# Kernel optimization log

Hardware: AMD Instinct MI355X
Metric: run time of the kernel (lower is better)

The kernel has to match this reference:

```python
import jax, jax.numpy as jnp
import numpy as np

N_NODES = 50000


def _gcn_conv(x, W, b, src, dst, norm, n_nodes):
    # x: [N, Fin], W: [Fin, Fout]
    h = x @ W                                   # [N, Fout]
    msg = h[src] * norm[:, None]                # [E+N, Fout] edge messages
    out = jax.ops.segment_sum(msg, dst, num_segments=n_nodes)
    return out + b


def reference(x, edge_index, W1, b1, W2, b2):
    n = x.shape[0]
    # add self-loops (PyG GCNConv default add_self_loops=True)
    loop = jnp.arange(n, dtype=edge_index.dtype)
    src = jnp.concatenate([edge_index[0], loop])
    dst = jnp.concatenate([edge_index[1], loop])
    # symmetric degree normalization: deg over destination with unit weights
    deg = jax.ops.segment_sum(jnp.ones_like(dst, dtype=x.dtype), dst, num_segments=n)
    dinv = jnp.where(deg > 0, jax.lax.rsqrt(deg), 0.0)
    norm = dinv[src] * dinv[dst]                # [E+N]
    h = _gcn_conv(x, W1, b1, src, dst, norm, n)
    h = jax.nn.relu(h)
    out = _gcn_conv(h, W2, b2, src, dst, norm, n)
    return out


def setup_inputs() -> dict:
    key = jax.random.key(0)
    k1, k2, k3, k4 = jax.random.split(key, 4)
    n, e, fin, hid, fout = N_NODES, 800000, 128, 128, 64
    x = jax.random.normal(k1, (n, fin), dtype=jnp.float32)
    edge_index = jax.random.randint(k2, (2, e), 0, n, dtype=jnp.int64)
    # Glorot-ish init for linear weights, zero bias (PyG default)
    W1 = jax.random.normal(k3, (fin, hid), dtype=jnp.float32) / np.sqrt(fin)
    b1 = jnp.zeros((hid,), dtype=jnp.float32)
    W2 = jax.random.normal(k4, (hid, fout), dtype=jnp.float32) / np.sqrt(hid)
    b2 = jnp.zeros((fout,), dtype=jnp.float32)
    return {"x": x, "edge_index": edge_index, "W1": W1, "b1": b1, "W2": W2, "b2": b2}
```

## Files before the change

### kernel.cpp

```cpp
#include <hip/hip_runtime.h>
#include <hip/hip_bf16.h>


constexpr int FIN = 128;
constexpr int HID = 128;
constexpr int FOUT = 64;
constexpr int CAP = 48;
constexpr int NPB = 98;
constexpr int BCAP = 3072;
constexpr int OVF_MAX = 65536;

typedef __attribute__((ext_vector_type(8))) short s16x8;
typedef __attribute__((ext_vector_type(4))) float f32x4;

static __device__ __forceinline__ float bf2f(__hip_bfloat16 v) { return __bfloat162float(v); }
static __device__ __forceinline__ float lo2f(unsigned u) { union { unsigned i; float f; } c; c.i = u << 16; return c.f; }
static __device__ __forceinline__ float hi2f(unsigned u) { union { unsigned i; float f; } c; c.i = u & 0xffff0000u; return c.f; }
static __device__ __forceinline__ unsigned short f2bfu(float f) {
    __hip_bfloat16 h = __float2bfloat16(f);
    union { __hip_bfloat16 h; unsigned short u; } c; c.h = h; return c.u;
}
static __device__ __forceinline__ unsigned pack2(float a, float b) {
    return (unsigned)f2bfu(a) | ((unsigned)f2bfu(b) << 16);
}
static __device__ __forceinline__ void acc_add(float* acc, uint4 v) {
    acc[0] += lo2f(v.x); acc[1] += hi2f(v.x);
    acc[2] += lo2f(v.y); acc[3] += hi2f(v.y);
    acc[4] += lo2f(v.z); acc[5] += hi2f(v.z);
    acc[6] += lo2f(v.w); acc[7] += hi2f(v.w);
}
static __device__ __forceinline__ void acc_fma(float* acc, uint4 v, float w) {
    acc[0] += w * lo2f(v.x); acc[1] += w * hi2f(v.x);
    acc[2] += w * lo2f(v.y); acc[3] += w * hi2f(v.y);
    acc[4] += w * lo2f(v.z); acc[5] += w * hi2f(v.z);
    acc[6] += w * lo2f(v.w); acc[7] += w * hi2f(v.w);
}

struct SW { int s; float w; };

__global__ __launch_bounds__(256) void k_detect(const unsigned* __restrict__ xw,
                                                const int* __restrict__ eiw,
                                                int E, int* __restrict__ flags,
                                                int* __restrict__ gcur,
                                                int* __restrict__ cnt, int N, int zero_cnt) {
    if (zero_cnt)
        for (long i = (long)blockIdx.x * 256 + threadIdx.x; i < N; i += (long)gridDim.x * 256)
            cnt[i] = 0;
    if (blockIdx.x != 0) return;
    for (int i = threadIdx.x; i < 514; i += 256) gcur[i] = 0;
    __shared__ int s_bf16like, s_oddnz;
    if (threadIdx.x == 0) { s_bf16like = 0; s_oddnz = 0; }
    __syncthreads();
    int c = 0;
    for (int i = threadIdx.x; i < 4096; i += 256) {
        unsigned ex = ((xw[i] & 0xffffu) >> 7) & 0xffu;
        if (ex >= 117u && ex <= 130u) c++;
    }
    atomicAdd(&s_bf16like, c);
    int nz = 0;
    for (int i = threadIdx.x; i < 2048; i += 256)
        if (eiw[2 * i + 1] != 0) nz++;
    atomicAdd(&s_oddnz, nz);
    __syncthreads();
    if (threadIdx.x == 0) {
        flags[0] = (s_bf16like < 2048) ? 1 : 0;
        flags[1] = (s_oddnz == 0) ? 1 : 0;
    }
}

__global__ __launch_bounds__(256) void k_mega(const void* __restrict__ Xp,
                                              const void* __restrict__ Wp,
                                              const int* __restrict__ ei, int E, int N,
                                              int nbuk, int GB,
                                              int* __restrict__ gcur,
                                              unsigned* __restrict__ pairs,
                                              int2* __restrict__ ovfA,
                                              int* __restrict__ ovfAcnt,
                                              __hip_bfloat16* __restrict__ G,
                                              const int* __restrict__ flags) {
    extern __shared__ __align__(16) char smem[];
    const int tid = threadIdx.x;
    if ((int)blockIdx.x < GB) {
        short* Wt = (short*)smem;
        const bool f32m = flags[0] != 0;
        for (int i = tid; i < 128 * 128; i += 256) {
            int k = i >> 7, n = i & 127;
            float wv = f32m ? ((const float*)Wp)[(long)k * 128 + n]
                            : bf2f(((const __hip_bfloat16*)Wp)[(long)k * 128 + n]);
            Wt[n * 136 + k] = (short)f2bfu(wv);
        }
        __syncthreads();
        const int w = tid >> 6, lane = tid & 63;
        const int m = lane & 15, quad = lane >> 4;
        const int rowA = blockIdx.x * 64 + w * 16 + m;
        const int rowc = rowA < N ? rowA : N - 1;
        s16x8 afr[4];
#pragma unroll
        for (int kc = 0; kc < 4; ++kc) {
            const int k0 = kc * 32 + quad * 8;
            if (!f32m) {
                afr[kc] = *(const s16x8*)((const __hip_bfloat16*)Xp + (long)rowc * 128 + k0);
            } else {
                const float* p = (const float*)Xp + (long)rowc * 128 + k0;
                s16x8 t;
#pragma unroll
                for (int j = 0; j < 8; ++j) t[j] = (short)f2bfu(p[j]);
                afr[kc] = t;
            }
        }
        const int rbase = blockIdx.x * 64 + w * 16 + quad * 4;
#pragma unroll
        for (int ct = 0; ct < 8; ++ct) {
            f32x4 acc = {0.f, 0.f, 0.f, 0.f};
#pragma unroll
            for (int kc = 0; kc < 4; ++kc) {
                s16x8 bfr = *(const s16x8*)&Wt[(ct * 16 + m) * 136 + kc * 32 + quad * 8];
                acc = __builtin_amdgcn_mfma_f32_16x16x32_bf16(afr[kc], bfr, acc, 0, 0, 0);
            }
            const int plane = ct >> 2;
            const int cp = (ct & 3) * 16 + m;
#pragma unroll
            for (int r = 0; r < 4; ++r) {
                int rr = rbase + r;
                if (rr < N)
                    G[(long)plane * N * 64 + (long)rr * 64 + cp] = __float2bfloat16(acc[r]);
            }
        }
    } else {
        int* hist = (int*)smem;
        int* gbase = hist + 512;
        const long base = (long)(blockIdx.x - GB) * 2048;
        const bool i64 = flags[1] != 0;
        int se[8], de[8];
        for (int b = tid; b < nbuk; b += 256) hist[b] = 0;
        __syncthreads();
#pragma unroll
        for (int j = 0; j < 8; ++j) {
            long i = base + j * 256 + tid;
            int s = 0, d = -1;
            if (i < E) {
                if (i64) { s = ((const int2*)ei)[i].x; d = ((const int2*)(ei + 2 * (long)E))[i].x; }
                else     { s = ei[i]; d = ei[(long)E + i]; }
                if ((unsigned)s >= (unsigned)N || (unsigned)d >= (unsigned)N) d = -1;
            }
            se[j] = s; de[j] = d;
            if (d >= 0) atomicAdd(&hist[d / NPB], 1);
        }
        __syncthreads();
        for (int b = tid; b < nbuk; b += 256) {
            int h = hist[b];
            gbase[b] = h > 0 ? atomicAdd(&gcur[b], h) : 0;
            hist[b] = 0;
        }
        __syncthreads();
#pragma unroll
        for (int j = 0; j < 8; ++j) {
            int d = de[j];
            if (d < 0) continue;
            int b = d / NPB;
            int p = gbase[b] + atomicAdd(&hist[b], 1);
            if (p < BCAP) {
                pairs[(long)b * BCAP + p] = ((unsigned)(d - b * NPB) << 16) | (unsigned)se[j];
            } else {
                int op = atomicAdd(ovfAcnt, 1);
                if (op < OVF_MAX) ovfA[op] = make_int2(d, se[j]);
            }
        }
    }
}

__global__ __launch_bounds__(256) void k_binB(const int* __restrict__ gcur,
                                              const unsigned* __restrict__ pairs,
                                              const int2* __restrict__ ovfA,
                                              const int* __restrict__ ovfAcnt,
                                              int* __restrict__ cnt,
                                              float* __restrict__ dinv,
                                              unsigned short* __restrict__ slots,
                                              int2* __restrict__ ovf2,
                                              int* __restrict__ ovf2cnt, int N) {
    __shared__ int cntL[NPB];
    __shared__ __align__(16) unsigned short slotsL[NPB * CAP];
    const int b = blockIdx.x;
    const int tid = threadIdx.x;
    const int d0 = b * NPB;
    const int nd = min(NPB, N - d0);
    if (nd <= 0) return;
    for (int i = tid; i < NPB; i += 256) cntL[i] = 0;
    __syncthreads();
    const int c = min(gcur[b], BCAP);
    const unsigned* pb = pairs + (long)b * BCAP;
    for (int i = tid; i < c; i += 256) {
        unsigned p = pb[i];
        int ld = p >> 16;
        int pos = atomicAdd(&cntL[ld], 1);
        if (pos < CAP) {
            slotsL[ld * CAP + pos] = (unsigned short)(p & 0xffffu);
        } else {
            int op = atomicAdd(ovf2cnt, 1);
            if (op < OVF_MAX) ovf2[op] = make_int2(d0 + ld, (int)(p & 0xffffu));
        }
    }
    int na = *ovfAcnt; na = na < OVF_MAX ? na : OVF_MAX;
    for (int i = tid; i < na; i += 256) {
        int2 p = ovfA[i];
        int ld = p.x - d0;
        if ((unsigned)ld < (unsigned)nd) {
            int pos = atomicAdd(&cntL[ld], 1);
            if (pos < CAP) {
                slotsL[ld * CAP + pos] = (unsigned short)p.y;
            } else {
                int op = atomicAdd(ovf2cnt, 1);
                if (op < OVF_MAX) ovf2[op] = p;
            }
        }
    }
    __syncthreads();
    for (int i = tid; i < nd; i += 256) {
        cnt[d0 + i] = cntL[i];
        dinv[d0 + i] = rsqrtf((float)(cntL[i] + 1));
    }
    const uint4* sv = (const uint4*)slotsL;
    uint4* gv = (uint4*)(slots + (long)d0 * CAP);
    const int total8 = (nd * CAP) >> 3;
    for (int i = tid; i < total8; i += 256) gv[i] = sv[i];
}

__global__ __launch_bounds__(256) void k_build_direct(const int* __restrict__ ei, int E, int N,
                                                      int* __restrict__ cnt,
                                                      int* __restrict__ slots,
                                                      int2* __restrict__ ovf2,
                                                      int* __restrict__ ovf2cnt,
                                                      const int* __restrict__ flags) {
    long i = (long)blockIdx.x * 256 + threadIdx.x;
    if (i >= E) return;
    int s, d;
    if (flags[1]) { s = ((const int2*)ei)[i].x; d = ((const int2*)(ei + 2 * (long)E))[i].x; }
    else          { s = ei[i]; d = ei[(long)E + i]; }
    if ((unsigned)s >= (unsigned)N || (unsigned)d >= (unsigned)N) return;
    int pos = atomicAdd(&cnt[d], 1);
    if (pos < CAP) {
        slots[(long)d * CAP + pos] = s;
    } else {
        int op = atomicAdd(ovf2cnt, 1);
        if (op < OVF_MAX) ovf2[op] = make_int2(d, s);
    }
}

template<int CT, int SPLIT>
__global__ __launch_bounds__(256) void k_gemm(const void* __restrict__ Xp, int x_follows_flag,
                                              const void* __restrict__ Wp,
                                              const int* __restrict__ cnt,
                                              __hip_bfloat16* __restrict__ G,
                                              const int* __restrict__ flags, int N) {
    constexpr int C = CT * 16;
    __shared__ __align__(16) short Wt[C * 136];
    const bool f32m = flags[0] != 0;
    const bool xf32 = (x_follows_flag != 0) && f32m;
    const int tid = threadIdx.x;
    for (int i = tid; i < 128 * C; i += 256) {
        int k = i / C, n = i % C;
        float wv = f32m ? ((const float*)Wp)[(long)k * C + n]
                        : bf2f(((const __hip_bfloat16*)Wp)[(long)k * C + n]);
        Wt[n * 136 + k] = (short)f2bfu(wv);
    }
    __syncthreads();
    const int w = tid >> 6, lane = tid & 63;
    const int m = lane & 15, quad = lane >> 4;
    const int rowA = blockIdx.x * 64 + w * 16 + m;
    const int rowc = rowA < N ? rowA : N - 1;
    s16x8 afr[4];
#pragma unroll
    for (int kc = 0; kc < 4; ++kc) {
        const int k0 = kc * 32 + quad * 8;
        if (!xf32) {
            afr[kc] = *(const s16x8*)((const __hip_bfloat16*)Xp + (long)rowc * 128 + k0);
        } else {
            const float* p = (const float*)Xp + (long)rowc * 128 + k0;
            s16x8 t;
#pragma unroll
            for (int j = 0; j < 8; ++j) t[j] = (short)f2bfu(p[j]);
            afr[kc] = t;
        }
    }
    const int rbase = blockIdx.x * 64 + w * 16 + quad * 4;
    float dv[4];
#pragma unroll
    for (int r = 0; r < 4; ++r) {
        int rr = min(rbase + r, N - 1);
        dv[r] = rsqrtf((float)(cnt[rr] + 1));
    }
#pragma unroll
    for (int ct = 0; ct < CT; ++ct) {
        f32x4 acc = {0.f, 0.f, 0.f, 0.f};
#pragma unroll
        for (int kc = 0; kc < 4; ++kc) {
            s16x8 bfr = *(const s16x8*)&Wt[(ct * 16 + m) * 136 + kc * 32 + quad * 8];
            acc = __builtin_amdgcn_mfma_f32_16x16x32_bf16(afr[kc], bfr, acc, 0, 0, 0);
        }
#pragma unroll
        for (int r = 0; r < 4; ++r) {
            int rr = rbase + r;
            if (rr < N) {
                long off;
                if (SPLIT) {
                    const int plane = ct / (CT / 2);
                    const int cp = (ct % (CT / 2)) * 16 + m;
                    off = (long)plane * N * (C / 2) + (long)rr * (C / 2) + cp;
                } else {
                    off = (long)rr * C + ct * 16 + m;
                }
                G[off] = __float2bfloat16(dv[r] * acc[r]);
            }
        }
    }
}

__global__ __launch_bounds__(256) void k_gather1b(const __hip_bfloat16* __restrict__ G,
                                                  const int* __restrict__ cnt,
                                                  const float* __restrict__ dinv,
                                                  const unsigned short* __restrict__ slots,
                                                  const int2* __restrict__ ovf2,
                                                  const int* __restrict__ ovf2cnt,
                                                  const void* __restrict__ b1,
                                                  __hip_bfloat16* __restrict__ h1,
                                                  const int* __restrict__ flags, int N) {
    __shared__ int cntL[32];
    __shared__ float wsL[32];
    __shared__ __align__(16) SW swL[32 * 49];
    const int tid = threadIdx.x;
    const int n0 = blockIdx.x * 32;
    const int nd = min(32, N - n0);
    for (int i = tid; i < nd; i += 256) {
        cntL[i] = cnt[n0 + i];
        wsL[i] = dinv[n0 + i];
    }
    __syncthreads();
    for (int j = tid; j < 32 * CAP; j += 256) {
        const int ni = j / CAP, sl = j - ni * CAP;
        if (ni < nd) {
            const int mm = min(cntL[ni], CAP);
            if (sl < mm) {
                const int s = slots[(long)(n0 + ni) * CAP + sl];
                swL[ni * 49 + sl].s = s;
                swL[ni * 49 + sl].w = dinv[s];
            }
        }
    }
    __syncthreads();
    const int grp = tid >> 3, lane = tid & 7;
    if (grp >= nd) return;
    const int node = n0 + grp;
    const int cd = cntL[grp];
    const int m = cd < CAP ? cd : CAP;
    const float wself = wsL[grp];
    const SW* sw = &swL[grp * 49];
    const bool f32m = flags[0] != 0;
    for (int P = 0; P < 2; ++P) {
        const __hip_bfloat16* Gp = G + (long)P * N * 64;
        float acc[8] = {0, 0, 0, 0, 0, 0, 0, 0};
        acc_fma(acc, ((const uint4*)(Gp + (long)node * 64))[lane], wself);
        int i = 0;
        for (; i + 7 < m; i += 8) {
            SW a0 = sw[i], a1 = sw[i + 1], a2 = sw[i + 2], a3 = sw[i + 3];
            SW a4 = sw[i + 4], a5 = sw[i + 5], a6 = sw[i + 6], a7 = sw[i + 7];
            uint4 v0 = ((const uint4*)(Gp + (long)a0.s * 64))[lane];
            uint4 v1 = ((const uint4*)(Gp + (long)a1.s * 64))[lane];
            uint4 v2 = ((const uint4*)(Gp + (long)a2.s * 64))[lane];
            uint4 v3 = ((const uint4*)(Gp + (long)a3.s * 64))[lane];
            uint4 v4 = ((const uint4*)(Gp + (long)a4.s * 64))[lane];
            uint4 v5 = ((const uint4*)(Gp + (long)a5.s * 64))[lane];
            uint4 v6 = ((const uint4*)(Gp + (long)a6.s * 64))[lane];
            uint4 v7 = ((const uint4*)(Gp + (long)a7.s * 64))[lane];
            acc_fma(acc, v0, a0.w); acc_fma(acc, v1, a1.w);
            acc_fma(acc, v2, a2.w); acc_fma(acc, v3, a3.w);
            acc_fma(acc, v4, a4.w); acc_fma(acc, v5, a5.w);
            acc_fma(acc, v6, a6.w); acc_fma(acc, v7, a7.w);
        }
        for (; i + 3 < m; i += 4) {
            SW a0 = sw[i], a1 = sw[i + 1], a2 = sw[i + 2], a3 = sw[i + 3];
            uint4 v0 = ((const uint4*)(Gp + (long)a0.s * 64))[lane];
            uint4 v1 = ((const uint4*)(Gp + (long)a1.s * 64))[lane];
            uint4 v2 = ((const uint4*)(Gp + (long)a2.s * 64))[lane];
            uint4 v3 = ((const uint4*)(Gp + (long)a3.s * 64))[lane];
            acc_fma(acc, v0, a0.w); acc_fma(acc, v1, a1.w);
            acc_fma(acc, v2, a2.w); acc_fma(acc, v3, a3.w);
        }
        for (; i < m; ++i) {
            SW a = sw[i];
            acc_fma(acc, ((const uint4*)(Gp + (long)a.s * 64))[lane], a.w);
        }
        if (cd > CAP) {
            int oc = *ovf2cnt; oc = oc < OVF_MAX ? oc : OVF_MAX;
            for (int j = 0; j < oc; ++j)
                if (ovf2[j].x == node) {
                    int s0 = ovf2[j].y;
                    acc_fma(acc, ((const uint4*)(Gp + (long)s0 * 64))[lane], dinv[s0]);
                }
        }
        const int c0 = P * 64 + lane * 8;
        float bv[8];
        if (f32m) {
            const float4* bp = (const float4*)((const float*)b1 + c0);
            float4 b0 = bp[0], b1v = bp[1];
            bv[0] = b0.x; bv[1] = b0.y; bv[2] = b0.z; bv[3] = b0.w;
            bv[4] = b1v.x; bv[5] = b1v.y; bv[6] = b1v.z; bv[7] = b1v.w;
        } else {
            uint4 b = *(const uint4*)((const __hip_bfloat16*)b1 + c0);
            bv[0] = lo2f(b.x); bv[1] = hi2f(b.x); bv[2] = lo2f(b.y); bv[3] = hi2f(b.y);
            bv[4] = lo2f(b.z); bv[5] = hi2f(b.z); bv[6] = lo2f(b.w); bv[7] = hi2f(b.w);
        }
        float o[8];
#pragma unroll
        for (int c = 0; c < 8; ++c) {
            float v = wself * acc[c] + bv[c];
            o[c] = v > 0.f ? v : 0.f;
        }
        uint4 pv = { pack2(o[0], o[1]), pack2(o[2], o[3]), pack2(o[4], o[5]), pack2(o[6], o[7]) };
        ((uint4*)(h1 + (long)node * 128 + P * 64))[lane] = pv;
    }
}

template<int F, int LAYER1, typename ST>
__global__ __launch_bounds__(256) void k_gather(const __hip_bfloat16* __restrict__ G,
                                                const int* __restrict__ cnt,
                                                const ST* __restrict__ slots,
                                                const int2* __restrict__ ovf2,
                                                const int* __restrict__ ovf2cnt,
                                                const void* __restrict__ bias,
                                                void* __restrict__ outp,
                                                const int* __restrict__ flags, int N) {
    constexpr int L = F / 8;
    constexpr int NODES = 256 / L;
    const int tid = threadIdx.x;
    const int grp = tid / L, lane = tid % L;
    const int node = blockIdx.x * NODES + grp;
    if (node >= N) return;
    const int cd = cnt[node];
    const float wself = rsqrtf((float)(cd + 1));
    const int m = cd < CAP ? cd : CAP;
    const ST* sl = slots + (long)node * CAP;
    float acc[8] = {0, 0, 0, 0, 0, 0, 0, 0};
    acc_add(acc, ((const uint4*)(G + (long)node * F))[lane]);
    int i = 0;
    for (; i + 7 < m; i += 8) {
        int s0 = sl[i], s1 = sl[i + 1], s2 = sl[i + 2], s3 = sl[i + 3];
        int s4 = sl[i + 4], s5 = sl[i + 5], s6 = sl[i + 6], s7 = sl[i + 7];
        uint4 v0 = ((const uint4*)(G + (long)s0 * F))[lane];
        uint4 v1 = ((const uint4*)(G + (long)s1 * F))[lane];
        uint4 v2 = ((const uint4*)(G + (long)s2 * F))[lane];
        uint4 v3 = ((const uint4*)(G + (long)s3 * F))[lane];
        uint4 v4 = ((const uint4*)(G + (long)s4 * F))[lane];
        uint4 v5 = ((const uint4*)(G + (long)s5 * F))[lane];
        uint4 v6 = ((const uint4*)(G + (long)s6 * F))[lane];
        uint4 v7 = ((const uint4*)(G + (long)s7 * F))[lane];
        acc_add(acc, v0); acc_add(acc, v1); acc_add(acc, v2); acc_add(acc, v3);
        acc_add(acc, v4); acc_add(acc, v5); acc_add(acc, v6); acc_add(acc, v7);
    }
    for (; i + 3 < m; i += 4) {
        int s0 = sl[i], s1 = sl[i + 1], s2 = sl[i + 2], s3 = sl[i + 3];
        uint4 v0 = ((const uint4*)(G + (long)s0 * F))[lane];
        uint4 v1 = ((const uint4*)(G + (long)s1 * F))[lane];
        uint4 v2 = ((const uint4*)(G + (long)s2 * F))[lane];
        uint4 v3 = ((const uint4*)(G + (long)s3 * F))[lane];
        acc_add(acc, v0); acc_add(acc, v1); acc_add(acc, v2); acc_add(acc, v3);
    }
    for (; i < m; ++i)
        acc_add(acc, ((const uint4*)(G + (long)sl[i] * F))[lane]);
    if (cd > CAP) {
        int oc = *ovf2cnt; oc = oc < OVF_MAX ? oc : OVF_MAX;
        for (int j = 0; j < oc; ++j)
            if (ovf2[j].x == node)
                acc_add(acc, ((const uint4*)(G + (long)ovf2[j].y * F))[lane]);
    }
    const bool f32m = flags[0] != 0;
    const int c0 = lane * 8;
    float bv[8];
    if (f32m) {
        const float4* bp = (const float4*)((const float*)bias + c0);
        float4 b0 = bp[0], b1 = bp[1];
        bv[0] = b0.x; bv[1] = b0.y; bv[2] = b0.z; bv[3] = b0.w;
        bv[4] = b1.x; bv[5] = b1.y; bv[6] = b1.z; bv[7] = b1.w;
    } else {
        uint4 b = *(const uint4*)((const __hip_bfloat16*)bias + c0);
        bv[0] = lo2f(b.x); bv[1] = hi2f(b.x); bv[2] = lo2f(b.y); bv[3] = hi2f(b.y);
        bv[4] = lo2f(b.z); bv[5] = hi2f(b.z); bv[6] = lo2f(b.w); bv[7] = hi2f(b.w);
    }
    float o[8];
#pragma unroll
    for (int c = 0; c < 8; ++c) {
        float v = wself * acc[c] + bv[c];
        o[c] = (LAYER1 && v < 0.f) ? 0.f : v;
    }
    if (LAYER1 || !f32m) {
        uint4 pv = { pack2(o[0], o[1]), pack2(o[2], o[3]), pack2(o[4], o[5]), pack2(o[6], o[7]) };
        ((uint4*)outp)[(long)node * L + lane] = pv;
    } else {
        float4* op = (float4*)((float*)outp + (long)node * F + c0);
        op[0] = make_float4(o[0], o[1], o[2], o[3]);
        op[1] = make_float4(o[4], o[5], o[6], o[7]);
    }
}

extern "C" void kernel_launch(void* const* d_in, const int* in_sizes, int n_in,
                              void* d_out, int out_size, void* d_ws, size_t ws_size,
                              hipStream_t stream) {
    const void* x  = d_in[0];
    const int*  ei = (const int*)d_in[1];
    const void* W1 = d_in[2];
    const void* b1 = d_in[3];
    const void* W2 = d_in[4];
    const void* b2 = d_in[5];

    const int N = in_sizes[0] / FIN;
    const int E = in_sizes[1] / 2;
    const int nbuk = (N + NPB - 1) / NPB;

    char* ws = (char*)d_ws;
    int*   flags   = (int*)ws;
    int*   gcur    = (int*)(ws + 4096);
    int*   ovfAcnt = gcur + 512;
    int*   ovf2cnt = gcur + 513;
    int*   cnt     = (int*)(ws + 65536);
    float* dinv    = (float*)(ws + 266240);
    int2*  ovfA    = (int2*)(ws + 524288);
    int2*  ovf2    = (int2*)(ws + 1048576);
    unsigned short* slots16 = (unsigned short*)(ws + 2097152);
    int*   slots32 = (int*)(ws + 2097152);
    __hip_bfloat16* g  = (__hip_bfloat16*)(ws + 11730944);
    __hip_bfloat16* g2 = g;
    unsigned* pairs = (unsigned*)(ws + 24530944);
    __hip_bfloat16* h1 = (__hip_bfloat16*)(ws + 24530944);

    const int GB = (N + 63) / 64;
    const int AB = (E + 2047) / 2048;
    const int EB = (E + 255) / 256;

    if (N <= 65536 && nbuk <= 512) {
        k_detect<<<1, 256, 0, stream>>>((const unsigned*)x, ei, E, flags, gcur, cnt, N, 0);
        k_mega<<<GB + AB, 256, 34816, stream>>>(x, W1, ei, E, N, nbuk, GB,
                                                gcur, pairs, ovfA, ovfAcnt, g, flags);
        k_binB<<<nbuk, 256, 0, stream>>>(gcur, pairs, ovfA, ovfAcnt, cnt, dinv, slots16, ovf2, ovf2cnt, N);
        const int GBL = (N + 31) / 32;
        k_gather1b<<<GBL, 256, 0, stream>>>(g, cnt, dinv, slots16, ovf2, ovf2cnt, b1, h1, flags, N);
        k_gemm<4, 0><<<GB, 256, 0, stream>>>(h1, 0, W2, cnt, g2, flags, N);
        k_gather<64, 0, unsigned short><<<(N + 31) / 32, 256, 0, stream>>>(
            g2, cnt, slots16, ovf2, ovf2cnt, b2, d_out, flags, N);
    } else {
        k_detect<<<64, 256, 0, stream>>>((const unsigned*)x, ei, E, flags, gcur, cnt, N, 1);
        k_build_direct<<<EB, 256, 0, stream>>>(ei, E, N, cnt, slots32, ovf2, ovf2cnt, flags);
        k_gemm<8, 0><<<GB, 256, 0, stream>>>(x, 1, W1, cnt, g, flags, N);
        k_gather<128, 1, int><<<(N + 15) / 16, 256, 0, stream>>>(
            g, cnt, slots32, ovf2, ovf2cnt, b1, h1, flags, N);
        k_gemm<4, 0><<<GB, 256, 0, stream>>>(h1, 0, W2, cnt, g2, flags, N);
        k_gather<64, 0, int><<<(N + 31) / 32, 256, 0, stream>>>(
            g2, cnt, slots32, ovf2, ovf2cnt, b2, d_out, flags, N);
    }
}
```

Before: 190.9 us.

## Sort nodes by degree within buckets to balance gather wavefront work

The bin kernel now builds a per-bucket permutation that orders destination nodes by in-degree using a small shared-memory histogram and prefix sum. Both gather kernels process nodes in this permuted order, so the 8-lane groups in a wavefront see similar neighbor counts and lose less time to divergence. A new dedicated layer-2 gather stages slot indices in shared memory the way the layer-1 gather does. The bucket size grows from 98 to 128 nodes, which enlarges shared memory per bin block. It also adds an extra indirection through the permutation and scatters the output writes.

After: 193.9 us. About the same (+1.6%).

```diff
diff --git a/kernel.cpp b/kernel.cpp
--- a/kernel.cpp
+++ b/kernel.cpp
@@ -6,7 +6,7 @@
 constexpr int HID = 128;
 constexpr int FOUT = 64;
 constexpr int CAP = 48;
-constexpr int NPB = 98;
+constexpr int NPB = 128;
 constexpr int BCAP = 3072;
 constexpr int OVF_MAX = 65536;
 
@@ -176,16 +176,20 @@
                                               int* __restrict__ cnt,
                                               float* __restrict__ dinv,
                                               unsigned short* __restrict__ slots,
+                                              unsigned short* __restrict__ perm,
                                               int2* __restrict__ ovf2,
                                               int* __restrict__ ovf2cnt, int N) {
     __shared__ int cntL[NPB];
     __shared__ __align__(16) unsigned short slotsL[NPB * CAP];
+    __shared__ int h64[64], p64[64];
+    __shared__ unsigned short ordL[NPB];
     const int b = blockIdx.x;
     const int tid = threadIdx.x;
     const int d0 = b * NPB;
     const int nd = min(NPB, N - d0);
     if (nd <= 0) return;
     for (int i = tid; i < NPB; i += 256) cntL[i] = 0;
+    if (tid < 64) h64[tid] = 0;
     __syncthreads();
     const int c = min(gcur[b], BCAP);
     const unsigned* pb = pairs + (long)b * BCAP;
@@ -218,11 +222,26 @@
     for (int i = tid; i < nd; i += 256) {
         cnt[d0 + i] = cntL[i];
         dinv[d0 + i] = rsqrtf((float)(cntL[i] + 1));
+        atomicAdd(&h64[min(cntL[i], 63)], 1);
     }
     const uint4* sv = (const uint4*)slotsL;
     uint4* gv = (uint4*)(slots + (long)d0 * CAP);
     const int total8 = (nd * CAP) >> 3;
     for (int i = tid; i < total8; i += 256) gv[i] = sv[i];
+    __syncthreads();
+    if (tid == 0) {
+        int r = 0;
+        for (int bb = 0; bb < 64; ++bb) { p64[bb] = r; r += h64[bb]; }
+    }
+    __syncthreads();
+    for (int i = tid; i < nd; i += 256) {
+        int bb = min(cntL[i], 63);
+        int pos = atomicAdd(&p64[bb], 1);
+        ordL[pos] = (unsigned short)i;
+    }
+    __syncthreads();
+    for (int i = tid; i < nd; i += 256)
+        perm[d0 + i] = (unsigned short)(d0 + ordL[i]);
 }
 
 __global__ __launch_bounds__(256) void k_build_direct(const int* __restrict__ ei, int E, int N,
@@ -319,6 +338,7 @@
                                                   const int* __restrict__ cnt,
                                                   const float* __restrict__ dinv,
                                                   const unsigned short* __restrict__ slots,
+                                                  const unsigned short* __restrict__ perm,
                                                   const int2* __restrict__ ovf2,
                                                   const int* __restrict__ ovf2cnt,
                                                   const void* __restrict__ b1,
@@ -326,13 +346,16 @@
                                                   const int* __restrict__ flags, int N) {
     __shared__ int cntL[32];
     __shared__ float wsL[32];
+    __shared__ unsigned short ndL[32];
     __shared__ __align__(16) SW swL[32 * 49];
     const int tid = threadIdx.x;
     const int n0 = blockIdx.x * 32;
     const int nd = min(32, N - n0);
     for (int i = tid; i < nd; i += 256) {
-        cntL[i] = cnt[n0 + i];
-        wsL[i] = dinv[n0 + i];
+        const int nodeG = perm[n0 + i];
+        ndL[i] = (unsigned short)nodeG;
+        cntL[i] = cnt[nodeG];
+        wsL[i] = dinv[nodeG];
     }
     __syncthreads();
     for (int j = tid; j < 32 * CAP; j += 256) {
@@ -340,7 +363,7 @@
         if (ni < nd) {
             const int mm = min(cntL[ni], CAP);
             if (sl < mm) {
-                const int s = slots[(long)(n0 + ni) * CAP + sl];
+                const int s = slots[(long)ndL[ni] * CAP + sl];
                 swL[ni * 49 + sl].s = s;
                 swL[ni * 49 + sl].w = dinv[s];
             }
@@ -349,7 +372,7 @@
     __syncthreads();
     const int grp = tid >> 3, lane = tid & 7;
     if (grp >= nd) return;
-    const int node = n0 + grp;
+    const int node = ndL[grp];
     const int cd = cntL[grp];
     const int m = cd < CAP ? cd : CAP;
     const float wself = wsL[grp];
@@ -417,6 +440,104 @@
         }
         uint4 pv = { pack2(o[0], o[1]), pack2(o[2], o[3]), pack2(o[4], o[5]), pack2(o[6], o[7]) };
         ((uint4*)(h1 + (long)node * 128 + P * 64))[lane] = pv;
+    }
+}
+
+__global__ __launch_bounds__(256) void k_gather2b(const __hip_bfloat16* __restrict__ G,
+                                                  const int* __restrict__ cnt,
+                                                  const float* __restrict__ dinv,
+                                                  const unsigned short* __restrict__ slots,
+                                                  const unsigned short* __restrict__ perm,
+                                                  const int2* __restrict__ ovf2,
+                                                  const int* __restrict__ ovf2cnt,
+                                                  const void* __restrict__ bias,
+                                                  void* __restrict__ outp,
+                                                  const int* __restrict__ flags, int N) {
+    __shared__ int cntL[32];
+    __shared__ float wsL[32];
+    __shared__ unsigned short ndL[32];
+    __shared__ unsigned short slL[32 * 49];
+    const int tid = threadIdx.x;
+    const int n0 = blockIdx.x * 32;
+    const int nd = min(32, N - n0);
+    for (int i = tid; i < nd; i += 256) {
+        const int nodeG = perm[n0 + i];
+        ndL[i] = (unsigned short)nodeG;
+        cntL[i] = cnt[nodeG];
+        wsL[i] = dinv[nodeG];
+    }
+    __syncthreads();
+    for (int j = tid; j < 32 * CAP; j += 256) {
+        const int ni = j / CAP, sl = j - ni * CAP;
+        if (ni < nd) {
+            const int mm = min(cntL[ni], CAP);
+            if (sl < mm) slL[ni * 49 + sl] = slots[(long)ndL[ni] * CAP + sl];
+        }
+    }
+    __syncthreads();
+    const int grp = tid >> 3, lane = tid & 7;
+    if (grp >= nd) return;
+    const int node = ndL[grp];
+    const int cd = cntL[grp];
+    const int m = cd < CAP ? cd : CAP;
+    const float wself = wsL[grp];
+    const unsigned short* sl = &slL[grp * 49];
+    const bool f32m = flags[0] != 0;
+    float acc[8] = {0, 0, 0, 0, 0, 0, 0, 0};
+    acc_add(acc, ((const uint4*)(G + (long)node * 64))[lane]);
+    int i = 0;
+    for (; i + 7 < m; i += 8) {
+        int s0 = sl[i], s1 = sl[i + 1], s2 = sl[i + 2], s3 = sl[i + 3];
+        int s4 = sl[i + 4], s5 = sl[i + 5], s6 = sl[i + 6], s7 = sl[i + 7];
+        uint4 v0 = ((const uint4*)(G + (long)s0 * 64))[lane];
+        uint4 v1 = ((const uint4*)(G + (long)s1 * 64))[lane];
+        uint4 v2 = ((const uint4*)(G + (long)s2 * 64))[lane];
+        uint4 v3 = ((const uint4*)(G + (long)s3 * 64))[lane];
+        uint4 v4 = ((const uint4*)(G + (long)s4 * 64))[lane];
+        uint4 v5 = ((const uint4*)(G + (long)s5 * 64))[lane];
+        uint4 v6 = ((const uint4*)(G + (long)s6 * 64))[lane];
+        uint4 v7 = ((const uint4*)(G + (long)s7 * 64))[lane];
+        acc_add(acc, v0); acc_add(acc, v1); acc_add(acc, v2); acc_add(acc, v3);
+        acc_add(acc, v4); acc_add(acc, v5); acc_add(acc, v6); acc_add(acc, v7);
+    }
+    for (; i + 3 < m; i += 4) {
+        int s0 = sl[i], s1 = sl[i + 1], s2 = sl[i + 2], s3 = sl[i + 3];
+        uint4 v0 = ((const uint4*)(G + (long)s0 * 64))[lane];
+        uint4 v1 = ((const uint4*)(G + (long)s1 * 64))[lane];
+        uint4 v2 = ((const uint4*)(G + (long)s2 * 64))[lane];
+        uint4 v3 = ((const uint4*)(G + (long)s3 * 64))[lane];
+        acc_add(acc, v0); acc_add(acc, v1); acc_add(acc, v2); acc_add(acc, v3);
+    }
+    for (; i < m; ++i)
+        acc_add(acc, ((const uint4*)(G + (long)sl[i] * 64))[lane]);
+    if (cd > CAP) {
+        int oc = *ovf2cnt; oc = oc < OVF_MAX ? oc : OVF_MAX;
+        for (int j = 0; j < oc; ++j)
+            if (ovf2[j].x == node)
+                acc_add(acc, ((const uint4*)(G + (long)ovf2[j].y * 64))[lane]);
+    }
+    const int c0 = lane * 8;
+    float bv[8];
+    if (f32m) {
+        const float4* bp = (const float4*)((const float*)bias + c0);
+        float4 b0 = bp[0], b1 = bp[1];
+        bv[0] = b0.x; bv[1] = b0.y; bv[2] = b0.z; bv[3] = b0.w;
+        bv[4] = b1.x; bv[5] = b1.y; bv[6] = b1.z; bv[7] = b1.w;
+    } else {
+        uint4 b = *(const uint4*)((const __hip_bfloat16*)bias + c0);
+        bv[0] = lo2f(b.x); bv[1] = hi2f(b.x); bv[2] = lo2f(b.y); bv[3] = hi2f(b.y);
+        bv[4] = lo2f(b.z); bv[5] = hi2f(b.z); bv[6] = lo2f(b.w); bv[7] = hi2f(b.w);
+    }
+    float o[8];
+#pragma unroll
+    for (int c = 0; c < 8; ++c) o[c] = wself * acc[c] + bv[c];
+    if (!f32m) {
+        uint4 pv = { pack2(o[0], o[1]), pack2(o[2], o[3]), pack2(o[4], o[5]), pack2(o[6], o[7]) };
+        ((uint4*)outp)[(long)node * 8 + lane] = pv;
+    } else {
+        float4* op = (float4*)((float*)outp + (long)node * FOUT + c0);
+        op[0] = make_float4(o[0], o[1], o[2], o[3]);
+        op[1] = make_float4(o[4], o[5], o[6], o[7]);
     }
 }
 
@@ -524,6 +645,7 @@
     float* dinv    = (float*)(ws + 266240);
     int2*  ovfA    = (int2*)(ws + 524288);
     int2*  ovf2    = (int2*)(ws + 1048576);
+    unsigned short* perm = (unsigned short*)(ws + 1572864);
     unsigned short* slots16 = (unsigned short*)(ws + 2097152);
     int*   slots32 = (int*)(ws + 2097152);
     __hip_bfloat16* g  = (__hip_bfloat16*)(ws + 11730944);
@@ -539,12 +661,12 @@
         k_detect<<<1, 256, 0, stream>>>((const unsigned*)x, ei, E, flags, gcur, cnt, N, 0);
         k_mega<<<GB + AB, 256, 34816, stream>>>(x, W1, ei, E, N, nbuk, GB,
                                                 gcur, pairs, ovfA, ovfAcnt, g, flags);
-        k_binB<<<nbuk, 256, 0, stream>>>(gcur, pairs, ovfA, ovfAcnt, cnt, dinv, slots16, ovf2, ovf2cnt, N);
+        k_binB<<<nbuk, 256, 0, stream>>>(gcur, pairs, ovfA, ovfAcnt, cnt, dinv, slots16, perm,
+                                         ovf2, ovf2cnt, N);
         const int GBL = (N + 31) / 32;
-        k_gather1b<<<GBL, 256, 0, stream>>>(g, cnt, dinv, slots16, ovf2, ovf2cnt, b1, h1, flags, N);
+        k_gather1b<<<GBL, 256, 0, stream>>>(g, cnt, dinv, slots16, perm, ovf2, ovf2cnt, b1, h1, flags, N);
         k_gemm<4, 0><<<GB, 256, 0, stream>>>(h1, 0, W2, cnt, g2, flags, N);
-        k_gather<64, 0, unsigned short><<<(N + 31) / 32, 256, 0, stream>>>(
-            g2, cnt, slots16, ovf2, ovf2cnt, b2, d_out, flags, N);
+        k_gather2b<<<GBL, 256, 0, stream>>>(g2, cnt, dinv, slots16, perm, ovf2, ovf2cnt, b2, d_out, flags, N);
     } else {
         k_detect<<<64, 256, 0, stream>>>((const unsigned*)x, ei, E, flags, gcur, cnt, N, 1);
         k_build_direct<<<EB, 256, 0, stream>>>(ei, E, N, cnt, slots32, ovf2, ovf2cnt, flags);
```

## Stage binned edge pairs in LDS for coalesced writes; use packed float2 accumulation

Applied to the files above, without the earlier changes.

The edge-binning phase now computes a per-block prefix sum of bucket counts, scatters the packed (dst,src) pairs into a local LDS buffer grouped by bucket, then writes them to global memory in contiguous runs found by binary search. The goal is to replace scattered per-edge global stores with mostly coalesced ones. The bucket size NPB rises from 98 to 128, so there are fewer, larger buckets. The gather accumulators switch to float2 vectors so the compiler can emit packed FMA/add instructions. The serial prefix scan on one thread and the per-element binary search add latency, and larger buckets change how much work and LDS each binB block handles.

Measured after the change: 202.9 us. +6.3%, slower.

```diff
diff --git a/kernel.cpp b/kernel.cpp
--- a/kernel.cpp
+++ b/kernel.cpp
@@ -6,12 +6,13 @@
 constexpr int HID = 128;
 constexpr int FOUT = 64;
 constexpr int CAP = 48;
-constexpr int NPB = 98;
+constexpr int NPB = 128;
 constexpr int BCAP = 3072;
 constexpr int OVF_MAX = 65536;
 
 typedef __attribute__((ext_vector_type(8))) short s16x8;
 typedef __attribute__((ext_vector_type(4))) float f32x4;
+typedef __attribute__((ext_vector_type(2))) float f32x2;
 
 static __device__ __forceinline__ float bf2f(__hip_bfloat16 v) { return __bfloat162float(v); }
 static __device__ __forceinline__ float lo2f(unsigned u) { union { unsigned i; float f; } c; c.i = u << 16; return c.f; }
@@ -23,17 +24,19 @@
 static __device__ __forceinline__ unsigned pack2(float a, float b) {
     return (unsigned)f2bfu(a) | ((unsigned)f2bfu(b) << 16);
 }
-static __device__ __forceinline__ void acc_add(float* acc, uint4 v) {
-    acc[0] += lo2f(v.x); acc[1] += hi2f(v.x);
-    acc[2] += lo2f(v.y); acc[3] += hi2f(v.y);
-    acc[4] += lo2f(v.z); acc[5] += hi2f(v.z);
-    acc[6] += lo2f(v.w); acc[7] += hi2f(v.w);
-}
-static __device__ __forceinline__ void acc_fma(float* acc, uint4 v, float w) {
-    acc[0] += w * lo2f(v.x); acc[1] += w * hi2f(v.x);
-    acc[2] += w * lo2f(v.y); acc[3] += w * hi2f(v.y);
-    acc[4] += w * lo2f(v.z); acc[5] += w * hi2f(v.z);
-    acc[6] += w * lo2f(v.w); acc[7] += w * hi2f(v.w);
+static __device__ __forceinline__ f32x2 unpk(unsigned u) {
+    union { unsigned i; float f; } a, b;
+    a.i = u << 16; b.i = u & 0xffff0000u;
+    f32x2 r; r[0] = a.f; r[1] = b.f; return r;
+}
+static __device__ __forceinline__ void acc_add(f32x2* acc, uint4 v) {
+    acc[0] += unpk(v.x); acc[1] += unpk(v.y);
+    acc[2] += unpk(v.z); acc[3] += unpk(v.w);
+}
+static __device__ __forceinline__ void acc_fma(f32x2* acc, uint4 v, float w) {
+    f32x2 ws; ws[0] = w; ws[1] = w;
+    acc[0] += ws * unpk(v.x); acc[1] += ws * unpk(v.y);
+    acc[2] += ws * unpk(v.z); acc[3] += ws * unpk(v.w);
 }
 
 struct SW { int s; float w; };
@@ -127,8 +130,11 @@
             }
         }
     } else {
-        int* hist = (int*)smem;
+        int* hist  = (int*)smem;
         int* gbase = hist + 512;
+        int* lofs  = gbase + 512;
+        int* cur   = lofs + 513;
+        unsigned* buf = (unsigned*)(cur + 512);
         const long base = (long)(blockIdx.x - GB) * 2048;
         const bool i64 = flags[1] != 0;
         int se[8], de[8];
@@ -147,10 +153,16 @@
             if (d >= 0) atomicAdd(&hist[d / NPB], 1);
         }
         __syncthreads();
+        if (tid == 0) {
+            int r = 0;
+            for (int b = 0; b < nbuk; ++b) { lofs[b] = r; r += hist[b]; }
+            lofs[nbuk] = r;
+        }
+        __syncthreads();
         for (int b = tid; b < nbuk; b += 256) {
+            cur[b] = lofs[b];
             int h = hist[b];
             gbase[b] = h > 0 ? atomicAdd(&gcur[b], h) : 0;
-            hist[b] = 0;
         }
         __syncthreads();
 #pragma unroll
@@ -158,12 +170,23 @@
             int d = de[j];
             if (d < 0) continue;
             int b = d / NPB;
-            int p = gbase[b] + atomicAdd(&hist[b], 1);
-            if (p < BCAP) {
-                pairs[(long)b * BCAP + p] = ((unsigned)(d - b * NPB) << 16) | (unsigned)se[j];
+            int lp = atomicAdd(&cur[b], 1);
+            buf[lp] = ((unsigned)(d - b * NPB) << 16) | (unsigned)se[j];
+        }
+        __syncthreads();
+        const int total = lofs[nbuk];
+        for (int i = tid; i < total; i += 256) {
+            int lo = 0, hi = nbuk;
+            while (hi - lo > 1) { int mid = (lo + hi) >> 1; if (lofs[mid] <= i) lo = mid; else hi = mid; }
+            const int b = lo;
+            const unsigned val = buf[i];
+            const int gp = gbase[b] + (i - lofs[b]);
+            if (gp < BCAP) {
+                pairs[(long)b * BCAP + gp] = val;
             } else {
                 int op = atomicAdd(ovfAcnt, 1);
-                if (op < OVF_MAX) ovfA[op] = make_int2(d, se[j]);
+                if (op < OVF_MAX)
+                    ovfA[op] = make_int2(b * NPB + (int)(val >> 16), (int)(val & 0xffffu));
             }
         }
     }
@@ -357,8 +380,9 @@
     const bool f32m = flags[0] != 0;
     for (int P = 0; P < 2; ++P) {
         const __hip_bfloat16* Gp = G + (long)P * N * 64;
-        float acc[8] = {0, 0, 0, 0, 0, 0, 0, 0};
-        acc_fma(acc, ((const uint4*)(Gp + (long)node * 64))[lane], wself);
+        f32x2 acc2[4] = {};
+        float* acc = (float*)acc2;
+        acc_fma(acc2, ((const uint4*)(Gp + (long)node * 64))[lane], wself);
         int i = 0;
         for (; i + 7 < m; i += 8) {
             SW a0 = sw[i], a1 = sw[i + 1], a2 = sw[i + 2], a3 = sw[i + 3];
@@ -371,10 +395,10 @@
             uint4 v5 = ((const uint4*)(Gp + (long)a5.s * 64))[lane];
             uint4 v6 = ((const uint4*)(Gp + (long)a6.s * 64))[lane];
             uint4 v7 = ((const uint4*)(Gp + (long)a7.s * 64))[lane];
-            acc_fma(acc, v0, a0.w); acc_fma(acc, v1, a1.w);
-            acc_fma(acc, v2, a2.w); acc_fma(acc, v3, a3.w);
-            acc_fma(acc, v4, a4.w); acc_fma(acc, v5, a5.w);
-            acc_fma(acc, v6, a6.w); acc_fma(acc, v7, a7.w);
+            acc_fma(acc2, v0, a0.w); acc_fma(acc2, v1, a1.w);
+            acc_fma(acc2, v2, a2.w); acc_fma(acc2, v3, a3.w);
+            acc_fma(acc2, v4, a4.w); acc_fma(acc2, v5, a5.w);
+            acc_fma(acc2, v6, a6.w); acc_fma(acc2, v7, a7.w);
         }
         for (; i + 3 < m; i += 4) {
             SW a0 = sw[i], a1 = sw[i + 1], a2 = sw[i + 2], a3 = sw[i + 3];
@@ -382,19 +406,19 @@
             uint4 v1 = ((const uint4*)(Gp + (long)a1.s * 64))[lane];
             uint4 v2 = ((const uint4*)(Gp + (long)a2.s * 64))[lane];
             uint4 v3 = ((const uint4*)(Gp + (long)a3.s * 64))[lane];
-            acc_fma(acc, v0, a0.w); acc_fma(acc, v1, a1.w);
-            acc_fma(acc, v2, a2.w); acc_fma(acc, v3, a3.w);
+            acc_fma(acc2, v0, a0.w); acc_fma(acc2, v1, a1.w);
+            acc_fma(acc2, v2, a2.w); acc_fma(acc2, v3, a3.w);
         }
         for (; i < m; ++i) {
             SW a = sw[i];
-            acc_fma(acc, ((const uint4*)(Gp + (long)a.s * 64))[lane], a.w);
+            acc_fma(acc2, ((const uint4*)(Gp + (long)a.s * 64))[lane], a.w);
         }
         if (cd > CAP) {
             int oc = *ovf2cnt; oc = oc < OVF_MAX ? oc : OVF_MAX;
             for (int j = 0; j < oc; ++j)
                 if (ovf2[j].x == node) {
                     int s0 = ovf2[j].y;
-                    acc_fma(acc, ((const uint4*)(Gp + (long)s0 * 64))[lane], dinv[s0]);
+                    acc_fma(acc2, ((const uint4*)(Gp + (long)s0 * 64))[lane], dinv[s0]);
                 }
         }
         const int c0 = P * 64 + lane * 8;
@@ -439,8 +463,9 @@
     const float wself = rsqrtf((float)(cd + 1));
     const int m = cd < CAP ? cd : CAP;
     const ST* sl = slots + (long)node * CAP;
-    float acc[8] = {0, 0, 0, 0, 0, 0, 0, 0};
-    acc_add(acc, ((const uint4*)(G + (long)node * F))[lane]);
+    f32x2 acc2[4] = {};
+    float* acc = (float*)acc2;
+    acc_add(acc2, ((const uint4*)(G + (long)node * F))[lane]);
     int i = 0;
     for (; i + 7 < m; i += 8) {
         int s0 = sl[i], s1 = sl[i + 1], s2 = sl[i + 2], s3 = sl[i + 3];
@@ -453,8 +478,8 @@
         uint4 v5 = ((const uint4*)(G + (long)s5 * F))[lane];
         uint4 v6 = ((const uint4*)(G + (long)s6 * F))[lane];
         uint4 v7 = ((const uint4*)(G + (long)s7 * F))[lane];
-        acc_add(acc, v0); acc_add(acc, v1); acc_add(acc, v2); acc_add(acc, v3);
-        acc_add(acc, v4); acc_add(acc, v5); acc_add(acc, v6); acc_add(acc, v7);
+        acc_add(acc2, v0); acc_add(acc2, v1); acc_add(acc2, v2); acc_add(acc2, v3);
+        acc_add(acc2, v4); acc_add(acc2, v5); acc_add(acc2, v6); acc_add(acc2, v7);
     }
     for (; i + 3 < m; i += 4) {
         int s0 = sl[i], s1 = sl[i + 1], s2 = sl[i + 2], s3 = sl[i + 3];
@@ -462,15 +487,15 @@
         uint4 v1 = ((const uint4*)(G + (long)s1 * F))[lane];
         uint4 v2 = ((const uint4*)(G + (long)s2 * F))[lane];
         uint4 v3 = ((const uint4*)(G + (long)s3 * F))[lane];
-        acc_add(acc, v0); acc_add(acc, v1); acc_add(acc, v2); acc_add(acc, v3);
+        acc_add(acc2, v0); acc_add(acc2, v1); acc_add(acc2, v2); acc_add(acc2, v3);
     }
     for (; i < m; ++i)
-        acc_add(acc, ((const uint4*)(G + (long)sl[i] * F))[lane]);
+        acc_add(acc2, ((const uint4*)(G + (long)sl[i] * F))[lane]);
     if (cd > CAP) {
         int oc = *ovf2cnt; oc = oc < OVF_MAX ? oc : OVF_MAX;
         for (int j = 0; j < oc; ++j)
             if (ovf2[j].x == node)
-                acc_add(acc, ((const uint4*)(G + (long)ovf2[j].y * F))[lane]);
+                acc_add(acc2, ((const uint4*)(G + (long)ovf2[j].y * F))[lane]);
     }
     const bool f32m = flags[0] != 0;
     const int c0 = lane * 8;
@@ -553,6 +578,6 @@
             g, cnt, slots32, ovf2, ovf2cnt, b1, h1, flags, N);
         k_gemm<4, 0><<<GB, 256, 0, stream>>>(h1, 0, W2, cnt, g2, flags, N);
         k_gather<64, 0, int><<<(N + 31) / 32, 256, 0, stream>>>(
-            g2, cnt, slots32, ovf2, ovf2cnt, b2, d_out, flags, N);
-    }
-}
+            g2, cnt, slots16 ? (const int*)slots32 : (const int*)slots32, ovf2, ovf2cnt, b2, d_out, flags, N);
+    }
+}
```
